# Kernel optimization log

Hardware: AMD Instinct MI355X
Metric: run time of the kernel (lower is better)

## Reference

```python
import jax, jax.numpy as jnp
import numpy as np

N_NODES = 100000
N_EDGES = 1600000
IN_CH = 128
HID = 128   # 2 * out_channels
OUT_CH = 64


def setup_inputs() -> dict:
    key = jax.random.key(0)
    k1, k2, k3, k4, k5, k6 = jax.random.split(key, 6)
    x = jax.random.normal(k1, (N_NODES, IN_CH), dtype=jnp.float32)
    edge_index = jax.random.randint(k2, (2, N_EDGES), 0, N_NODES, dtype=jnp.int64)
    W1 = jax.random.normal(k3, (IN_CH, HID), dtype=jnp.float32) / np.sqrt(IN_CH)
    b1 = jax.random.normal(k4, (HID,), dtype=jnp.float32) * 0.01
    W2 = jax.random.normal(k5, (HID, OUT_CH), dtype=jnp.float32) / np.sqrt(HID)
    b2 = jax.random.normal(k6, (OUT_CH,), dtype=jnp.float32) * 0.01
    return {"x": x, "edge_index": edge_index, "W1": W1, "b1": b1, "W2": W2, "b2": b2}


def _gcn_layer(x, src, dst, norm, W, b, n_nodes):
    # GCNConv: linear transform, then normalized scatter-add aggregation + bias
    h = x @ W                                   # [N, d_out]
    msg = h[src] * norm[:, None]                # gather + edge normalize, [E+N, d_out]
    out = jax.ops.segment_sum(msg, dst, num_segments=n_nodes)
    return out + b


def reference(x, edge_index, W1, b1, W2, b2):
    n = x.shape[0]
    loop = jnp.arange(n, dtype=edge_index.dtype)
    # add self-loops (PyG GCNConv default)
    src = jnp.concatenate([edge_index[0], loop])
    dst = jnp.concatenate([edge_index[1], loop])
    # symmetric normalization deg^-1/2[src] * deg^-1/2[dst]
    deg = jax.ops.segment_sum(jnp.ones_like(dst, x.dtype), dst, num_segments=n)
    dinv = jnp.where(deg > 0, jax.lax.rsqrt(deg), 0.0)
    norm = dinv[src] * dinv[dst]

    h = jax.nn.relu(_gcn_layer(x, src, dst, norm, W1, b1, n))
    out = jax.nn.relu(_gcn_layer(h, src, dst, norm, W2, b2, n))
    return out
```

## Files before the change

kernel.cpp:

```cpp
#include <hip/hip_runtime.h>
#include <hip/hip_fp16.h>

typedef _Float16 f16x8 __attribute__((ext_vector_type(8)));
typedef float f32x4 __attribute__((ext_vector_type(4)));

#define BSH 9
#define BSZ 512
#define CAP 12288

__global__ __launch_bounds__(256) void passA(const int* __restrict__ ei,
                                             int* __restrict__ bcount, int E, int NB) {
  __shared__ int hist[256];
  int t = threadIdx.x;
  hist[t] = 0;
  __syncthreads();
  for (int e = blockIdx.x * 256 + t; e < E; e += gridDim.x * 256)
    atomicAdd(&hist[ei[E + e] >> BSH], 1);
  __syncthreads();
  if (t < NB && hist[t]) atomicAdd(&bcount[t], hist[t]);
}

__global__ __launch_bounds__(256) void scanB(const int* __restrict__ bcount,
                                             int* __restrict__ bstart,
                                             int* __restrict__ bfill, int NB, int E) {
  __shared__ int s[256];
  int t = threadIdx.x;
  int v = (t < NB) ? bcount[t] : 0;
  s[t] = v;
  __syncthreads();
  for (int off = 1; off < 256; off <<= 1) {
    int add = (t >= off) ? s[t - off] : 0;
    __syncthreads();
    s[t] += add;
    __syncthreads();
  }
  if (t < NB) {
    int ex = s[t] - v;
    bstart[t] = ex;
    bfill[t] = ex;
  }
  if (t == 0) bstart[NB] = E;
}

template <int NC, int NWC, bool IN_F16, bool SCALE>
__device__ __forceinline__ void gemm_mfma_body(
    const void* __restrict__ Xv, const float* __restrict__ W,
    const float* __restrict__ dinv, _Float16* __restrict__ G, int nrows, int bid,
    _Float16* Bs) {
  int t = threadIdx.x;
  {
    int n = t % NC;
    int kh = (t / NC) * (NC / 2);
    constexpr int NBLK = (NC / 2) / 8;
#pragma unroll
    for (int b = 0; b < NBLK; ++b) {
      f16x8 tmp;
#pragma unroll
      for (int j = 0; j < 8; ++j)
        tmp[j] = (_Float16)W[(size_t)(kh + b * 8 + j) * NC + n];
      *(f16x8*)(&Bs[n * 136 + kh + b * 8]) = tmp;
    }
  }
  __syncthreads();

  int w = t >> 6, lane = t & 63;
  int m = lane & 15, q = lane >> 4;
  int wr = (w / NWC) * 64, wc = (w % NWC) * 64;
  int row0 = bid * ((4 / NWC) * 64);

  f32x4 acc[4][4];
#pragma unroll
  for (int rt = 0; rt < 4; ++rt)
#pragma unroll
    for (int ct = 0; ct < 4; ++ct)
#pragma unroll
      for (int qq = 0; qq < 4; ++qq) acc[rt][ct][qq] = 0.f;

#pragma unroll
  for (int kc = 0; kc < 4; ++kc) {
    int kbase = kc * 32 + q * 8;
    f16x8 af[4];
#pragma unroll
    for (int rt = 0; rt < 4; ++rt) {
      int row = row0 + wr + rt * 16 + m;
      if constexpr (IN_F16) {
        f16x8 a = {0, 0, 0, 0, 0, 0, 0, 0};
        if (row < nrows) a = *(const f16x8*)((const _Float16*)Xv + (size_t)row * 128 + kbase);
        af[rt] = a;
      } else {
        float4 x0 = {0, 0, 0, 0}, x1 = {0, 0, 0, 0};
        if (row < nrows) {
          const float* Xf = (const float*)Xv;
          x0 = *(const float4*)(Xf + (size_t)row * 128 + kbase);
          x1 = *(const float4*)(Xf + (size_t)row * 128 + kbase + 4);
        }
        f16x8 a;
        a[0] = (_Float16)x0.x; a[1] = (_Float16)x0.y;
        a[2] = (_Float16)x0.z; a[3] = (_Float16)x0.w;
        a[4] = (_Float16)x1.x; a[5] = (_Float16)x1.y;
        a[6] = (_Float16)x1.z; a[7] = (_Float16)x1.w;
        af[rt] = a;
      }
    }
    f16x8 bf[4];
#pragma unroll
    for (int ct = 0; ct < 4; ++ct) {
      int n = wc + ct * 16 + m;
      bf[ct] = *(f16x8*)(&Bs[n * 136 + kbase]);
    }
#pragma unroll
    for (int rt = 0; rt < 4; ++rt)
#pragma unroll
      for (int ct = 0; ct < 4; ++ct)
        acc[rt][ct] = __builtin_amdgcn_mfma_f32_16x16x32_f16(af[rt], bf[ct],
                                                             acc[rt][ct], 0, 0, 0);
  }
#pragma unroll
  for (int rt = 0; rt < 4; ++rt) {
#pragma unroll
    for (int r = 0; r < 4; ++r) {
      int row = row0 + wr + rt * 16 + q * 4 + r;
      if (row < nrows) {
        float d = SCALE ? dinv[row] : 1.f;
#pragma unroll
        for (int ct = 0; ct < 4; ++ct) {
          int col = wc + ct * 16 + m;
          G[(size_t)row * NC + col] = (_Float16)(acc[rt][ct][r] * d);
        }
      }
    }
  }
}

__global__ __launch_bounds__(256) void fused_gemm_passB(
    const float* __restrict__ X, const float* __restrict__ W1,
    _Float16* __restrict__ G, int nrows, int GB,
    const int* __restrict__ ei, int* __restrict__ bfill,
    unsigned int* __restrict__ pairs, int E, int PB) {
  __shared__ char smem[128 * 136 * 2];
  int g = blockIdx.x;
  int M2 = 2 * (GB < PB ? GB : PB);
  bool is_gemm;
  int bid;
  if (g < M2) { is_gemm = (g & 1) == 0; bid = g >> 1; }
  else        { is_gemm = (GB > PB);    bid = g - M2 + (GB < PB ? GB : PB); }
  if (is_gemm) {
    gemm_mfma_body<128, 2, false, false>(X, W1, nullptr, G, nrows, bid,
                                         (_Float16*)smem);
  } else {
    int* hist = (int*)smem;
    int* gbase = (int*)(smem + 1024);
    int t = threadIdx.x;
    hist[t] = 0;
    __syncthreads();
    int d[8], s[8], lp[8], bb[8];
    int base = bid * 2048;
#pragma unroll
    for (int u = 0; u < 8; ++u) {
      int e = base + u * 256 + t;
      if (e < E) {
        d[u] = ei[E + e];
        s[u] = ei[e];
        bb[u] = d[u] >> BSH;
        lp[u] = atomicAdd(&hist[bb[u]], 1);
      } else {
        bb[u] = -1;
      }
    }
    __syncthreads();
    if (hist[t]) gbase[t] = atomicAdd(&bfill[t], hist[t]);
    __syncthreads();
#pragma unroll
    for (int u = 0; u < 8; ++u)
      if (bb[u] >= 0)
        pairs[gbase[bb[u]] + lp[u]] =
            ((unsigned int)(d[u] & (BSZ - 1)) << 17) | (unsigned int)s[u];
  }
}

__global__ __launch_bounds__(256) void gemm2_mfma(const _Float16* __restrict__ X,
                                                  const float* __restrict__ W,
                                                  const float* __restrict__ dinv,
                                                  _Float16* __restrict__ G, int nrows) {
  __shared__ _Float16 Bs[64 * 136];
  gemm_mfma_body<64, 1, true, true>(X, W, dinv, G, nrows, blockIdx.x, Bs);
}

__global__ __launch_bounds__(512) void passC(const unsigned int* __restrict__ pairs,
                                             const int* __restrict__ bstart,
                                             int* __restrict__ rowstart,
                                             int* __restrict__ deg,
                                             float* __restrict__ dinv,
                                             int* __restrict__ csr, int N) {
  __shared__ int hcnt[BSZ];
  __shared__ int lfill[BSZ];
  __shared__ int ss[512];
  __shared__ int lcsr[CAP];
  int b = blockIdx.x;
  int t = threadIdx.x;
  int lo = bstart[b], hi = bstart[b + 1];
  int cnt = hi - lo;
  int nbase = b << BSH;
  hcnt[t] = 0;
  __syncthreads();
  for (int k = lo + t; k < hi; k += 512)
    atomicAdd(&hcnt[(pairs[k] >> 17) & (BSZ - 1)], 1);
  __syncthreads();
  int v = hcnt[t];
  ss[t] = v;
  __syncthreads();
  for (int off = 1; off < 512; off <<= 1) {
    int add = (t >= off) ? ss[t - off] : 0;
    __syncthreads();
    ss[t] += add;
    __syncthreads();
  }
  int ex = ss[t] - v;
  lfill[t] = ex;
  int node = nbase + t;
  if (node < N) {
    rowstart[node] = lo + ex;
    deg[node] = v;
    dinv[node] = rsqrtf((float)(v + 1));
  }
  __syncthreads();
  bool fits = (cnt <= CAP);
  for (int k = lo + t; k < hi; k += 512) {
    unsigned int p = pairs[k];
    int pos = atomicAdd(&lfill[(p >> 17) & (BSZ - 1)], 1);
    int src = (int)(p & 0x1FFFFu);
    if (fits) lcsr[pos] = src;
    else      csr[lo + pos] = src;
  }
  __syncthreads();
  if (fits)
    for (int k = t; k < cnt; k += 512) csr[lo + k] = lcsr[k];
}

__global__ __launch_bounds__(256) void agg128(
    const __half* __restrict__ G, const int* __restrict__ csr,
    const int* __restrict__ rowstart, const int* __restrict__ deg,
    const float* __restrict__ dinv, const float* __restrict__ bias,
    __half* __restrict__ out, int n) {
  int wid = blockIdx.x * 4 + (threadIdx.x >> 6);
  if (wid >= n) return;
  int i = __builtin_amdgcn_readfirstlane(wid);
  int lane = threadIdx.x & 63;
  const __half2* Gp = (const __half2*)G;
  float di = dinv[i];
  float2 g = __half22float2(Gp[(size_t)i * 64 + lane]);
  float2 a = {di * g.x, di * g.y};
  int s = rowstart[i];
  int d = deg[i];
  int cnt = d < 64 ? d : 64;
  int myidx = 0;
  if (lane < cnt) myidx = csr[s + lane];
  int k = 0;
  for (; k + 3 < cnt; k += 4) {
    int s0 = __builtin_amdgcn_readfirstlane(__shfl(myidx, k));
    int s1 = __builtin_amdgcn_readfirstlane(__shfl(myidx, k + 1));
    int s2 = __builtin_amdgcn_readfirstlane(__shfl(myidx, k + 2));
    int s3 = __builtin_amdgcn_readfirstlane(__shfl(myidx, k + 3));
    float w0 = dinv[s0], w1 = dinv[s1], w2 = dinv[s2], w3 = dinv[s3];
    float2 v0 = __half22float2(Gp[(size_t)s0 * 64 + lane]);
    float2 v1 = __half22float2(Gp[(size_t)s1 * 64 + lane]);
    float2 v2 = __half22float2(Gp[(size_t)s2 * 64 + lane]);
    float2 v3 = __half22float2(Gp[(size_t)s3 * 64 + lane]);
    a.x = fmaf(w0, v0.x, a.x); a.y = fmaf(w0, v0.y, a.y);
    a.x = fmaf(w1, v1.x, a.x); a.y = fmaf(w1, v1.y, a.y);
    a.x = fmaf(w2, v2.x, a.x); a.y = fmaf(w2, v2.y, a.y);
    a.x = fmaf(w3, v3.x, a.x); a.y = fmaf(w3, v3.y, a.y);
  }
  for (; k < cnt; ++k) {
    int s0 = __builtin_amdgcn_readfirstlane(__shfl(myidx, k));
    float w0 = dinv[s0];
    float2 v0 = __half22float2(Gp[(size_t)s0 * 64 + lane]);
    a.x = fmaf(w0, v0.x, a.x); a.y = fmaf(w0, v0.y, a.y);
  }
  for (int j = s + 64; j < s + d; ++j) {
    int s0 = __builtin_amdgcn_readfirstlane(csr[j]);
    float w0 = dinv[s0];
    float2 v0 = __half22float2(Gp[(size_t)s0 * 64 + lane]);
    a.x = fmaf(w0, v0.x, a.x); a.y = fmaf(w0, v0.y, a.y);
  }
  float2 b = ((const float2*)bias)[lane];
  float ox = fmaxf(fmaf(di, a.x, b.x), 0.f);
  float oy = fmaxf(fmaf(di, a.y, b.y), 0.f);
  ((__half2*)out)[(size_t)i * 64 + lane] = __floats2half2_rn(ox, oy);
}

__global__ __launch_bounds__(256) void agg64(
    const __half* __restrict__ G, const int* __restrict__ csr,
    const int* __restrict__ rowstart, const int* __restrict__ deg,
    const float* __restrict__ dinv, const float* __restrict__ bias,
    float* __restrict__ out, int n) {
  int wid = blockIdx.x * 4 + (threadIdx.x >> 6);
  if (wid >= n) return;
  int i = __builtin_amdgcn_readfirstlane(wid);
  int lane = threadIdx.x & 63;
  float a = __half2float(G[(size_t)i * 64 + lane]);
  int s = rowstart[i];
  int d = deg[i];
  int cnt = d < 64 ? d : 64;
  int myidx = 0;
  if (lane < cnt) myidx = csr[s + lane];
  int k = 0;
  for (; k + 3 < cnt; k += 4) {
    int s0 = __builtin_amdgcn_readfirstlane(__shfl(myidx, k));
    int s1 = __builtin_amdgcn_readfirstlane(__shfl(myidx, k + 1));
    int s2 = __builtin_amdgcn_readfirstlane(__shfl(myidx, k + 2));
    int s3 = __builtin_amdgcn_readfirstlane(__shfl(myidx, k + 3));
    float v0 = __half2float(G[(size_t)s0 * 64 + lane]);
    float v1 = __half2float(G[(size_t)s1 * 64 + lane]);
    float v2 = __half2float(G[(size_t)s2 * 64 + lane]);
    float v3 = __half2float(G[(size_t)s3 * 64 + lane]);
    a += (v0 + v1) + (v2 + v3);
  }
  for (; k < cnt; ++k) {
    int s0 = __builtin_amdgcn_readfirstlane(__shfl(myidx, k));
    a += __half2float(G[(size_t)s0 * 64 + lane]);
  }
  for (int j = s + 64; j < s + d; ++j) {
    int s0 = __builtin_amdgcn_readfirstlane(csr[j]);
    a += __half2float(G[(size_t)s0 * 64 + lane]);
  }
  float o = fmaxf(fmaf(dinv[i], a, bias[lane]), 0.f);
  out[(size_t)i * 64 + lane] = o;
}

extern "C" void kernel_launch(void* const* d_in, const int* in_sizes, int n_in,
                              void* d_out, int out_size, void* d_ws, size_t ws_size,
                              hipStream_t stream) {
  const float* x  = (const float*)d_in[0];
  const int*   ei = (const int*)d_in[1];
  const float* W1 = (const float*)d_in[2];
  const float* b1 = (const float*)d_in[3];
  const float* W2 = (const float*)d_in[4];
  const float* b2 = (const float*)d_in[5];
  float* out = (float*)d_out;

  const int N = in_sizes[0] / 128;
  const int E = in_sizes[1] / 2;
  const int NB = (N + BSZ - 1) >> BSH;

  char* base = (char*)d_ws;
  size_t off = 0;
  auto alloc = [&](size_t bytes) -> void* {
    void* p = base + off;
    off += (bytes + 255) & ~(size_t)255;
    return p;
  };
  int*          bcount   = (int*)alloc(256 * 4);
  int*          bstart   = (int*)alloc(260 * 4);
  int*          bfill    = (int*)alloc(256 * 4);
  int*          deg      = (int*)alloc((size_t)N * 4);
  int*          rowstart = (int*)alloc((size_t)N * 4);
  float*        dinv     = (float*)alloc((size_t)N * 4);
  int*          csr      = (int*)alloc((size_t)E * 4);
  unsigned int* pairs    = (unsigned int*)alloc((size_t)E * 4);
  __half*       g1       = (__half*)alloc((size_t)N * 128 * 2);
  __half*       x2       = (__half*)alloc((size_t)N * 128 * 2);

  hipMemsetAsync(bcount, 0, 256 * 4, stream);
  passA<<<512, 256, 0, stream>>>(ei, bcount, E, NB);
  scanB<<<1, 256, 0, stream>>>(bcount, bstart, bfill, NB, E);

  int GB = (N + 127) / 128;
  int PB = (E + 2047) / 2048;
  fused_gemm_passB<<<GB + PB, 256, 0, stream>>>(x, W1, (_Float16*)g1, N, GB, ei,
                                                bfill, pairs, E, PB);
  passC<<<NB, 512, 0, stream>>>(pairs, bstart, rowstart, deg, dinv, csr, N);

  agg128<<<(N + 3) / 4, 256, 0, stream>>>(g1, csr, rowstart, deg, dinv, b1, x2, N);
  int G2B = (N + 255) / 256;
  gemm2_mfma<<<G2B, 256, 0, stream>>>((const _Float16*)x2, W2, dinv,
                                      (_Float16*)g1, N);
  agg64<<<(N + 3) / 4, 256, 0, stream>>>(g1, csr, rowstart, deg, dinv, b2, out, N);
}
```

Baseline: 297.7 us.

## Shrink CSR buckets to 128 nodes, split agg64 across half-waves, simplify agg128 indexing

Node buckets shrink from 512 to 128 nodes, so there are about 782 bucket blocks and passC runs with 256 threads. The histograms in passA, scanB and passB grow to 1024 entries to match. agg128 now reads csr indices directly from memory instead of broadcasting them through wave shuffles. agg64 splits each wave into two 32-lane halves that gather two neighbors per half per step with half2 loads, then combines the halves with a shuffle; the second-layer GEMM also writes to a separate buffer. The aim is more parallelism in the CSR build and better memory throughput in the 64-wide gather, at the cost of more global atomics on bfill and scalar index loads.

```diff
diff --git a/kernel.cpp b/kernel.cpp
--- a/kernel.cpp
+++ b/kernel.cpp
@@ -4,31 +4,32 @@
 typedef _Float16 f16x8 __attribute__((ext_vector_type(8)));
 typedef float f32x4 __attribute__((ext_vector_type(4)));
 
-#define BSH 9
-#define BSZ 512
-#define CAP 12288
+#define BSH 7
+#define BSZ 128
+#define CAP 3072
 
 __global__ __launch_bounds__(256) void passA(const int* __restrict__ ei,
                                              int* __restrict__ bcount, int E, int NB) {
-  __shared__ int hist[256];
+  __shared__ int hist[1024];
   int t = threadIdx.x;
-  hist[t] = 0;
+  for (int j = t; j < 1024; j += 256) hist[j] = 0;
   __syncthreads();
   for (int e = blockIdx.x * 256 + t; e < E; e += gridDim.x * 256)
     atomicAdd(&hist[ei[E + e] >> BSH], 1);
   __syncthreads();
-  if (t < NB && hist[t]) atomicAdd(&bcount[t], hist[t]);
-}
-
-__global__ __launch_bounds__(256) void scanB(const int* __restrict__ bcount,
-                                             int* __restrict__ bstart,
-                                             int* __restrict__ bfill, int NB, int E) {
-  __shared__ int s[256];
+  for (int j = t; j < NB; j += 256)
+    if (hist[j]) atomicAdd(&bcount[j], hist[j]);
+}
+
+__global__ __launch_bounds__(1024) void scanB(const int* __restrict__ bcount,
+                                              int* __restrict__ bstart,
+                                              int* __restrict__ bfill, int NB, int E) {
+  __shared__ int s[1024];
   int t = threadIdx.x;
   int v = (t < NB) ? bcount[t] : 0;
   s[t] = v;
   __syncthreads();
-  for (int off = 1; off < 256; off <<= 1) {
+  for (int off = 1; off < 1024; off <<= 1) {
     int add = (t >= off) ? s[t - off] : 0;
     __syncthreads();
     s[t] += add;
@@ -149,9 +150,9 @@
                                          (_Float16*)smem);
   } else {
     int* hist = (int*)smem;
-    int* gbase = (int*)(smem + 1024);
+    int* gbase = (int*)(smem + 4096);
     int t = threadIdx.x;
-    hist[t] = 0;
+    for (int j = t; j < 1024; j += 256) hist[j] = 0;
     __syncthreads();
     int d[8], s[8], lp[8], bb[8];
     int base = bid * 2048;
@@ -168,7 +169,8 @@
       }
     }
     __syncthreads();
-    if (hist[t]) gbase[t] = atomicAdd(&bfill[t], hist[t]);
+    for (int j = t; j < 1024; j += 256)
+      if (hist[j]) gbase[j] = atomicAdd(&bfill[j], hist[j]);
     __syncthreads();
 #pragma unroll
     for (int u = 0; u < 8; ++u)
@@ -186,7 +188,7 @@
   gemm_mfma_body<64, 1, true, true>(X, W, dinv, G, nrows, blockIdx.x, Bs);
 }
 
-__global__ __launch_bounds__(512) void passC(const unsigned int* __restrict__ pairs,
+__global__ __launch_bounds__(256) void passC(const unsigned int* __restrict__ pairs,
                                              const int* __restrict__ bstart,
                                              int* __restrict__ rowstart,
                                              int* __restrict__ deg,
@@ -194,38 +196,43 @@
                                              int* __restrict__ csr, int N) {
   __shared__ int hcnt[BSZ];
   __shared__ int lfill[BSZ];
-  __shared__ int ss[512];
   __shared__ int lcsr[CAP];
   int b = blockIdx.x;
   int t = threadIdx.x;
   int lo = bstart[b], hi = bstart[b + 1];
   int cnt = hi - lo;
   int nbase = b << BSH;
-  hcnt[t] = 0;
-  __syncthreads();
-  for (int k = lo + t; k < hi; k += 512)
+  if (t < BSZ) hcnt[t] = 0;
+  __syncthreads();
+  for (int k = lo + t; k < hi; k += 256)
     atomicAdd(&hcnt[(pairs[k] >> 17) & (BSZ - 1)], 1);
   __syncthreads();
-  int v = hcnt[t];
-  ss[t] = v;
-  __syncthreads();
-  for (int off = 1; off < 512; off <<= 1) {
-    int add = (t >= off) ? ss[t - off] : 0;
-    __syncthreads();
-    ss[t] += add;
-    __syncthreads();
-  }
-  int ex = ss[t] - v;
-  lfill[t] = ex;
-  int node = nbase + t;
-  if (node < N) {
-    rowstart[node] = lo + ex;
-    deg[node] = v;
-    dinv[node] = rsqrtf((float)(v + 1));
+  int v = 0;
+  if (t < BSZ) {
+    v = hcnt[t];
+    lfill[t] = v;
+  }
+  __syncthreads();
+  for (int off = 1; off < BSZ; off <<= 1) {
+    int add = 0;
+    if (t < BSZ && t >= off) add = lfill[t - off];
+    __syncthreads();
+    if (t < BSZ) lfill[t] += add;
+    __syncthreads();
+  }
+  if (t < BSZ) {
+    int ex = lfill[t] - v;
+    int node = nbase + t;
+    if (node < N) {
+      rowstart[node] = lo + ex;
+      deg[node] = v;
+      dinv[node] = rsqrtf((float)(v + 1));
+    }
+    lfill[t] = ex;
   }
   __syncthreads();
   bool fits = (cnt <= CAP);
-  for (int k = lo + t; k < hi; k += 512) {
+  for (int k = lo + t; k < hi; k += 256) {
     unsigned int p = pairs[k];
     int pos = atomicAdd(&lfill[(p >> 17) & (BSZ - 1)], 1);
     int src = (int)(p & 0x1FFFFu);
@@ -234,7 +241,7 @@
   }
   __syncthreads();
   if (fits)
-    for (int k = t; k < cnt; k += 512) csr[lo + k] = lcsr[k];
+    for (int k = t; k < cnt; k += 256) csr[lo + k] = lcsr[k];
 }
 
 __global__ __launch_bounds__(256) void agg128(
@@ -252,15 +259,10 @@
   float2 a = {di * g.x, di * g.y};
   int s = rowstart[i];
   int d = deg[i];
-  int cnt = d < 64 ? d : 64;
-  int myidx = 0;
-  if (lane < cnt) myidx = csr[s + lane];
   int k = 0;
-  for (; k + 3 < cnt; k += 4) {
-    int s0 = __builtin_amdgcn_readfirstlane(__shfl(myidx, k));
-    int s1 = __builtin_amdgcn_readfirstlane(__shfl(myidx, k + 1));
-    int s2 = __builtin_amdgcn_readfirstlane(__shfl(myidx, k + 2));
-    int s3 = __builtin_amdgcn_readfirstlane(__shfl(myidx, k + 3));
+  for (; k + 3 < d; k += 4) {
+    int s0 = csr[s + k], s1 = csr[s + k + 1];
+    int s2 = csr[s + k + 2], s3 = csr[s + k + 3];
     float w0 = dinv[s0], w1 = dinv[s1], w2 = dinv[s2], w3 = dinv[s3];
     float2 v0 = __half22float2(Gp[(size_t)s0 * 64 + lane]);
     float2 v1 = __half22float2(Gp[(size_t)s1 * 64 + lane]);
@@ -271,14 +273,8 @@
     a.x = fmaf(w2, v2.x, a.x); a.y = fmaf(w2, v2.y, a.y);
     a.x = fmaf(w3, v3.x, a.x); a.y = fmaf(w3, v3.y, a.y);
   }
-  for (; k < cnt; ++k) {
-    int s0 = __builtin_amdgcn_readfirstlane(__shfl(myidx, k));
-    float w0 = dinv[s0];
-    float2 v0 = __half22float2(Gp[(size_t)s0 * 64 + lane]);
-    a.x = fmaf(w0, v0.x, a.x); a.y = fmaf(w0, v0.y, a.y);
-  }
-  for (int j = s + 64; j < s + d; ++j) {
-    int s0 = __builtin_amdgcn_readfirstlane(csr[j]);
+  for (; k < d; ++k) {
+    int s0 = csr[s + k];
     float w0 = dinv[s0];
     float2 v0 = __half22float2(Gp[(size_t)s0 * 64 + lane]);
     a.x = fmaf(w0, v0.x, a.x); a.y = fmaf(w0, v0.y, a.y);
@@ -298,34 +294,33 @@
   if (wid >= n) return;
   int i = __builtin_amdgcn_readfirstlane(wid);
   int lane = threadIdx.x & 63;
-  float a = __half2float(G[(size_t)i * 64 + lane]);
-  int s = rowstart[i];
+  int e2 = lane >> 5, f = lane & 31;
+  const __half2* Gp = (const __half2*)G;
+  int r0 = rowstart[i];
   int d = deg[i];
-  int cnt = d < 64 ? d : 64;
-  int myidx = 0;
-  if (lane < cnt) myidx = csr[s + lane];
-  int k = 0;
-  for (; k + 3 < cnt; k += 4) {
-    int s0 = __builtin_amdgcn_readfirstlane(__shfl(myidx, k));
-    int s1 = __builtin_amdgcn_readfirstlane(__shfl(myidx, k + 1));
-    int s2 = __builtin_amdgcn_readfirstlane(__shfl(myidx, k + 2));
-    int s3 = __builtin_amdgcn_readfirstlane(__shfl(myidx, k + 3));
-    float v0 = __half2float(G[(size_t)s0 * 64 + lane]);
-    float v1 = __half2float(G[(size_t)s1 * 64 + lane]);
-    float v2 = __half2float(G[(size_t)s2 * 64 + lane]);
-    float v3 = __half2float(G[(size_t)s3 * 64 + lane]);
-    a += (v0 + v1) + (v2 + v3);
-  }
-  for (; k < cnt; ++k) {
-    int s0 = __builtin_amdgcn_readfirstlane(__shfl(myidx, k));
-    a += __half2float(G[(size_t)s0 * 64 + lane]);
-  }
-  for (int j = s + 64; j < s + d; ++j) {
-    int s0 = __builtin_amdgcn_readfirstlane(csr[j]);
-    a += __half2float(G[(size_t)s0 * 64 + lane]);
-  }
-  float o = fmaxf(fmaf(dinv[i], a, bias[lane]), 0.f);
-  out[(size_t)i * 64 + lane] = o;
+  float2 acc = {0.f, 0.f};
+  for (int k = 0; k < d; k += 4) {
+    int kA = k + e2, kB = k + 2 + e2;
+    int iA = i, iB = i;
+    float wA = 0.f, wB = 0.f;
+    if (kA < d) { iA = csr[r0 + kA]; wA = 1.f; }
+    if (kB < d) { iB = csr[r0 + kB]; wB = 1.f; }
+    float2 vA = __half22float2(Gp[(size_t)iA * 32 + f]);
+    float2 vB = __half22float2(Gp[(size_t)iB * 32 + f]);
+    acc.x = fmaf(wA, vA.x, acc.x); acc.y = fmaf(wA, vA.y, acc.y);
+    acc.x = fmaf(wB, vB.x, acc.x); acc.y = fmaf(wB, vB.y, acc.y);
+  }
+  acc.x += __shfl_xor(acc.x, 32);
+  acc.y += __shfl_xor(acc.y, 32);
+  if (e2 == 0) {
+    float di = dinv[i];
+    float2 g = __half22float2(Gp[(size_t)i * 32 + f]);
+    float2 b = ((const float2*)bias)[f];
+    float2 o;
+    o.x = fmaxf(fmaf(di, g.x + acc.x, b.x), 0.f);
+    o.y = fmaxf(fmaf(di, g.y + acc.y, b.y), 0.f);
+    ((float2*)out)[(size_t)i * 32 + f] = o;
+  }
 }
 
 extern "C" void kernel_launch(void* const* d_in, const int* in_sizes, int n_in,
@@ -350,9 +345,9 @@
     off += (bytes + 255) & ~(size_t)255;
     return p;
   };
-  int*          bcount   = (int*)alloc(256 * 4);
-  int*          bstart   = (int*)alloc(260 * 4);
-  int*          bfill    = (int*)alloc(256 * 4);
+  int*          bcount   = (int*)alloc(1024 * 4);
+  int*          bstart   = (int*)alloc(1032 * 4);
+  int*          bfill    = (int*)alloc(1024 * 4);
   int*          deg      = (int*)alloc((size_t)N * 4);
   int*          rowstart = (int*)alloc((size_t)N * 4);
   float*        dinv     = (float*)alloc((size_t)N * 4);
@@ -360,20 +355,22 @@
   unsigned int* pairs    = (unsigned int*)alloc((size_t)E * 4);
   __half*       g1       = (__half*)alloc((size_t)N * 128 * 2);
   __half*       x2       = (__half*)alloc((size_t)N * 128 * 2);
-
-  hipMemsetAsync(bcount, 0, 256 * 4, stream);
+  __half*       g2       = (__half*)alloc((size_t)N * 64 * 2);
+
+  hipMemsetAsync(bcount, 0, 1024 * 4, stream);
   passA<<<512, 256, 0, stream>>>(ei, bcount, E, NB);
-  scanB<<<1, 256, 0, stream>>>(bcount, bstart, bfill, NB, E);
+  scanB<<<1, 1024, 0, stream>>>(bcount, bstart, bfill, NB, E);
 
   int GB = (N + 127) / 128;
   int PB = (E + 2047) / 2048;
   fused_gemm_passB<<<GB + PB, 256, 0, stream>>>(x, W1, (_Float16*)g1, N, GB, ei,
                                                 bfill, pairs, E, PB);
-  passC<<<NB, 512, 0, stream>>>(pairs, bstart, rowstart, deg, dinv, csr, N);
-
-  agg128<<<(N + 3) / 4, 256, 0, stream>>>(g1, csr, rowstart, deg, dinv, b1, x2, N);
+  passC<<<NB, 256, 0, stream>>>(pairs, bstart, rowstart, deg, dinv, csr, N);
+
+  int ng = (N + 3) / 4;
+  agg128<<<ng, 256, 0, stream>>>(g1, csr, rowstart, deg, dinv, b1, x2, N);
   int G2B = (N + 255) / 256;
   gemm2_mfma<<<G2B, 256, 0, stream>>>((const _Float16*)x2, W2, dinv,
-                                      (_Float16*)g1, N);
-  agg64<<<(N + 3) / 4, 256, 0, stream>>>(g1, csr, rowstart, deg, dinv, b2, out, N);
-}
+                                      (_Float16*)g2, N);
+  agg64<<<ng, 256, 0, stream>>>(g2, csr, rowstart, deg, dinv, b2, out, N);
+}
```

Result: slower. 311.6 us (+4.7%).
